# Kernel tuning notes

Measured on AMD Instinct MI355X. Metric: run time of the kernel, lower is better.

## Reference

```python
import jax, jax.numpy as jnp
import numpy as np

NUM_HEADS = 16


def setup_inputs() -> dict:
    key = jax.random.key(0)
    ks = jax.random.split(key, 5)
    B, L, D = 2, 2048, 1024
    x = jax.random.normal(ks[0], (B, L, D), dtype=jnp.float32)
    s = 1.0 / np.sqrt(D)
    Wqkv_w = jax.random.normal(ks[1], (3 * D, D), dtype=jnp.float32) * s
    Wqkv_b = jax.random.normal(ks[2], (3 * D,), dtype=jnp.float32) * 0.01
    out_w = jax.random.normal(ks[3], (D, D), dtype=jnp.float32) * s
    out_b = jax.random.normal(ks[4], (D,), dtype=jnp.float32) * 0.01
    return {"x": x, "Wqkv_w": Wqkv_w, "Wqkv_b": Wqkv_b, "out_w": out_w, "out_b": out_b}


def reference(x, Wqkv_w, Wqkv_b, out_w, out_b):
    B, L, D = x.shape
    H = NUM_HEADS
    d = D // H
    scale = 1.0 / np.sqrt(d).astype(np.float32)
    # qkv projection: torch Linear is x @ W^T + b
    qkv = x @ Wqkv_w.T + Wqkv_b                      # [B, L, 3D]
    qkv = qkv.reshape(B, L, 3, H, d)                 # (three h d) split
    qkv = jnp.transpose(qkv, (2, 0, 3, 1, 4))        # [3, B, H, L, d]
    q, k, v = qkv[0], qkv[1], qkv[2]
    k = k * scale
    # Linear-attention recurrence S_t = S_{t-1} + v_t k_t^T, y_t = S_t q_t
    # == causally-masked unnormalized attention: y_t = sum_{s<=t} (q_t.k_s) v_s
    scores = jnp.einsum('bhld,bhmd->bhlm', q, k)     # [B,H,L,L]
    causal = jnp.tril(jnp.ones((L, L), dtype=scores.dtype))
    y = jnp.einsum('bhlm,bhmd->bhld', scores * causal, v)  # [B,H,L,d]
    y = jnp.transpose(y, (0, 2, 1, 3)).reshape(B, L, D)    # b l (h d)
    return y @ out_w.T + out_b
```

## Files before the change

### kernel.cpp

```cpp
#include <hip/hip_runtime.h>


#define DEV __device__ __forceinline__

typedef __attribute__((ext_vector_type(8))) short bf16x8;
typedef __attribute__((ext_vector_type(4))) float f32x4;

DEV ushort f2bf(float f) {
  union { float f; unsigned u; } v; v.f = f;
  unsigned r = v.u + 0x7fffu + ((v.u >> 16) & 1u);
  return (ushort)(r >> 16);
}
DEV float bf2f(unsigned b) {
  union { unsigned u; float f; } v; v.u = (b & 0xffffu) << 16;
  return v.f;
}
DEV void glds16(const ushort* g, ushort* l) {
  __builtin_amdgcn_global_load_lds(
      (const __attribute__((address_space(1))) unsigned int*)g,
      (__attribute__((address_space(3))) unsigned int*)l, 16, 0, 0);
}

__global__ __launch_bounds__(256) void cvt_all(const float* __restrict__ x,
                                               const float* __restrict__ Ww,
                                               const float* __restrict__ Ow,
                                               ushort* __restrict__ xb,
                                               ushort* __restrict__ wqkvb,
                                               ushort* __restrict__ outwb) {
  int i = blockIdx.x * 256 + threadIdx.x;
  const float* src; ushort* dst; int off;
  if (i < 1048576)      { src = x;  dst = xb;    off = i; }
  else if (i < 1835008) { src = Ww; dst = wqkvb; off = i - 1048576; }
  else                  { src = Ow; dst = outwb; off = i - 1835008; }
  float4 v = ((const float4*)src)[off];
  ushort4 o;
  o.x = f2bf(v.x); o.y = f2bf(v.y); o.z = f2bf(v.z); o.w = f2bf(v.w);
  ((ushort4*)dst)[off] = o;
}

template <bool OUT_BF16, bool KSCALE>
__global__ __launch_bounds__(512, 2) void gemm_bt8(const ushort* __restrict__ A,
                                                   const ushort* __restrict__ Bw,
                                                   const float* __restrict__ bias,
                                                   void* __restrict__ Cout,
                                                   int M, int N, int K) {
  __shared__ __align__(16) ushort As[2][16384];
  __shared__ __align__(16) ushort Bs[2][16384];
  const int t = threadIdx.x;
  const int lane = t & 63, wid = t >> 6;
  const int quad = lane >> 4, l16 = lane & 15;
  const int wm2 = wid >> 2, wn4 = wid & 3;

  const int nwg = gridDim.x;
  const int bid = blockIdx.x;
  const int wg = (bid & 7) * (nwg >> 3) + (bid >> 3);
  const int nbx = N >> 8;
  const int bx = wg % nbx, by = wg / nbx;
  const int bm = by << 8, bn = bx << 8;

  const int srow = t >> 3;
  const int scol = ((t & 7) ^ (srow & 7)) << 3;
  const ushort* ag = A + (size_t)(bm + srow) * K + scol;
  const ushort* bg = Bw + (size_t)(bn + srow) * K + scol;
  const int NT = K >> 6;

  f32x4 acc[8][4];
  const f32x4 z = {0.f, 0.f, 0.f, 0.f};
#pragma unroll
  for (int i = 0; i < 8; ++i)
#pragma unroll
    for (int j = 0; j < 4; ++j) acc[i][j] = z;

  const int aRow = wm2 * 128 + l16;
  const int bRow = wn4 * 64 + l16;
  const int cxor = l16 & 7;

#define SG_A(bufi, kt, h, j) \
  glds16(ag + (size_t)((h)*128 + (j)*64) * K + ((kt) << 6), \
         &As[bufi][(h)*8192 + (j)*4096 + wid * 512])
#define SG_B(bufi, kt, h, j) \
  glds16(bg + (size_t)((h)*128 + (j)*64) * K + ((kt) << 6), \
         &Bs[bufi][(h)*8192 + (j)*4096 + wid * 512])
#define RD_A(bufi, mi, kc) \
  (*(const bf16x8*)&As[bufi][(aRow + (mi)*16) * 64 + ((((kc)*4 + quad) ^ cxor) << 3)])
#define RD_B(bufi, nj, kc) \
  (*(const bf16x8*)&Bs[bufi][(bRow + (nj)*16) * 64 + ((((kc)*4 + quad) ^ cxor) << 3)])

  SG_A(0, 0, 0, 0); SG_A(0, 0, 0, 1); SG_A(0, 0, 1, 0); SG_A(0, 0, 1, 1);
  SG_B(0, 0, 0, 0); SG_B(0, 0, 0, 1); SG_B(0, 0, 1, 0); SG_B(0, 0, 1, 1);
  asm volatile("s_waitcnt vmcnt(0)" ::: "memory");
  __builtin_amdgcn_s_barrier();

  bf16x8 bf[4][2], af[2][2];

#define LOAD_AF(rb, mi0) \
  af[0][0] = RD_A(rb, (mi0), 0); af[0][1] = RD_A(rb, (mi0), 1); \
  af[1][0] = RD_A(rb, (mi0) + 1, 0); af[1][1] = RD_A(rb, (mi0) + 1, 1);

#define MFMA16(mi0) \
  __builtin_amdgcn_s_setprio(1); \
  _Pragma("unroll") \
  for (int nj = 0; nj < 4; ++nj) { \
    acc[(mi0)][nj] = __builtin_amdgcn_mfma_f32_16x16x32_bf16(af[0][0], bf[nj][0], acc[(mi0)][nj], 0, 0, 0); \
    acc[(mi0)][nj] = __builtin_amdgcn_mfma_f32_16x16x32_bf16(af[0][1], bf[nj][1], acc[(mi0)][nj], 0, 0, 0); \
    acc[(mi0) + 1][nj] = __builtin_amdgcn_mfma_f32_16x16x32_bf16(af[1][0], bf[nj][0], acc[(mi0) + 1][nj], 0, 0, 0); \
    acc[(mi0) + 1][nj] = __builtin_amdgcn_mfma_f32_16x16x32_bf16(af[1][1], bf[nj][1], acc[(mi0) + 1][nj], 0, 0, 0); \
  } \
  __builtin_amdgcn_s_setprio(0);

#define HALFSTEP(rb, sb, stTile, doSt) do { \
    if (doSt) { SG_A(sb, stTile, 0, 0); SG_A(sb, stTile, 0, 1); \
                SG_A(sb, stTile, 1, 0); SG_A(sb, stTile, 1, 1); } \
    _Pragma("unroll") \
    for (int nj = 0; nj < 4; ++nj) { bf[nj][0] = RD_B(rb, nj, 0); bf[nj][1] = RD_B(rb, nj, 1); } \
    LOAD_AF(rb, 0); \
    __builtin_amdgcn_s_barrier(); \
    MFMA16(0); \
    __builtin_amdgcn_s_barrier(); \
    if (doSt) { SG_B(sb, stTile, 0, 0); SG_B(sb, stTile, 0, 1); } \
    LOAD_AF(rb, 2); \
    __builtin_amdgcn_s_barrier(); \
    MFMA16(2); \
    __builtin_amdgcn_s_barrier(); \
    if (doSt) { SG_B(sb, stTile, 1, 0); SG_B(sb, stTile, 1, 1); } \
    LOAD_AF(rb, 4); \
    __builtin_amdgcn_s_barrier(); \
    MFMA16(4); \
    __builtin_amdgcn_s_barrier(); \
    LOAD_AF(rb, 6); \
    __builtin_amdgcn_s_barrier(); \
    MFMA16(6); \
    asm volatile("s_waitcnt vmcnt(0)" ::: "memory"); \
    __builtin_amdgcn_s_barrier(); \
  } while (0)

  const int half = NT >> 1;
  for (int i = 0; i < half; ++i) {
    HALFSTEP(0, 1, 2 * i + 1, true);
    HALFSTEP(1, 0, 2 * i + 2, (i < half - 1));
  }

#undef HALFSTEP
#undef MFMA16
#undef LOAD_AF
#undef RD_A
#undef RD_B
#undef SG_A
#undef SG_B

#pragma unroll
  for (int mi = 0; mi < 8; ++mi)
#pragma unroll
    for (int nj = 0; nj < 4; ++nj) {
      const int col = bn + wn4 * 64 + nj * 16 + l16;
      const float bv = bias[col];
      float sc = 1.f;
      if (KSCALE) sc = ((col >> 10) == 1) ? 0.125f : 1.f;
#pragma unroll
      for (int r = 0; r < 4; ++r) {
        const int row = bm + wm2 * 128 + mi * 16 + quad * 4 + r;
        const float v = (acc[mi][nj][r] + bv) * sc;
        if (OUT_BF16)
          ((ushort*)Cout)[(size_t)row * N + col] = f2bf(v);
        else
          ((float*)Cout)[(size_t)row * N + col] = v;
      }
    }
}

__global__ __launch_bounds__(256) void gemm_out64(const ushort* __restrict__ A,
                                                  const ushort* __restrict__ Bw,
                                                  const float* __restrict__ bias,
                                                  float* __restrict__ C,
                                                  int M, int N, int K) {
  __shared__ ushort As[64 * 32];
  __shared__ ushort Bs[128 * 32];
  const int t = threadIdx.x;
  const int wid = t >> 6, lane = t & 63;
  const int quad = lane >> 4, l16 = lane & 15;
  const int bm = blockIdx.y * 64, bn = blockIdx.x * 128;
  const int wn = wid * 32;

  f32x4 acc[4][2];
  const f32x4 z = {0.f, 0.f, 0.f, 0.f};
#pragma unroll
  for (int i = 0; i < 4; ++i) { acc[i][0] = z; acc[i][1] = z; }

  const ushort* ag = A + (size_t)(bm + (t >> 2)) * K + ((t & 3) * 8);
  const ushort* bg = Bw + (size_t)(bn + (t >> 2)) * K + ((t & 3) * 8);
  ushort* asl = As + wid * 512;
  ushort* bsl = Bs + wid * 512;
  const size_t rowskip = (size_t)64 * K;

  for (int k0 = 0; k0 < K; k0 += 32) {
    glds16(ag + k0, asl);
    glds16(bg + k0, bsl);
    glds16(bg + k0 + rowskip, bsl + 2048);
    __syncthreads();
    bf16x8 af[4], bf[2];
#pragma unroll
    for (int i = 0; i < 4; ++i)
      af[i] = *(const bf16x8*)(As + (i * 16 + l16) * 32 + quad * 8);
#pragma unroll
    for (int j = 0; j < 2; ++j)
      bf[j] = *(const bf16x8*)(Bs + (wn + j * 16 + l16) * 32 + quad * 8);
#pragma unroll
    for (int i = 0; i < 4; ++i)
#pragma unroll
      for (int j = 0; j < 2; ++j)
        acc[i][j] = __builtin_amdgcn_mfma_f32_16x16x32_bf16(af[i], bf[j], acc[i][j], 0, 0, 0);
    __syncthreads();
  }

#pragma unroll
  for (int i = 0; i < 4; ++i)
#pragma unroll
    for (int j = 0; j < 2; ++j) {
      const int col = bn + wn + j * 16 + l16;
      const float bv = bias[col];
#pragma unroll
      for (int r = 0; r < 4; ++r) {
        const int row = bm + i * 16 + quad * 4 + r;
        C[(size_t)row * N + col] = acc[i][j][r] + bv;
      }
    }
}

__global__ __launch_bounds__(256) void kv_local(const ushort* __restrict__ qkv,
                                                float* __restrict__ mlocT) {
  const int c = blockIdx.x, bh = blockIdx.y;
  const int b = bh >> 4, hd = bh & 15;
  const int t = threadIdx.x;
  const int wid = t >> 6, lane = t & 63;
  const int quad = lane >> 4, l16 = lane & 15;
  __shared__ ushort kT[64 * 136];
  __shared__ ushort vT[64 * 136];

  {
    const int x = t & 127;
    const int isv = t >> 7;
    const int rp = x >> 1;
    const int half = (x & 1) * 32;
    const ushort* g0 = qkv + (size_t)(b * 2048 + c * 128 + 2 * rp) * 3072 +
                       1024 + isv * 1024 + hd * 64 + half;
    const ushort* g1 = g0 + 3072;
    ushort ta[32], tb[32];
#pragma unroll
    for (int q = 0; q < 4; ++q) {
      *(uint4*)(ta + q * 8) = *(const uint4*)(g0 + q * 8);
      *(uint4*)(tb + q * 8) = *(const uint4*)(g1 + q * 8);
    }
    ushort* dst = isv ? vT : kT;
#pragma unroll
    for (int j = 0; j < 32; ++j) {
      unsigned pk = (unsigned)ta[j] | ((unsigned)tb[j] << 16);
      *(unsigned*)(dst + (half + j) * 136 + 2 * rp) = pk;
    }
  }
  __syncthreads();

  const f32x4 z = {0.f, 0.f, 0.f, 0.f};
  f32x4 acc[4];
#pragma unroll
  for (int ct = 0; ct < 4; ++ct) acc[ct] = z;
#pragma unroll
  for (int kc = 0; kc < 4; ++kc) {
    bf16x8 afr = *(const bf16x8*)(vT + (wid * 16 + l16) * 136 + kc * 32 + quad * 8);
#pragma unroll
    for (int ct = 0; ct < 4; ++ct) {
      bf16x8 bfr = *(const bf16x8*)(kT + (ct * 16 + l16) * 136 + kc * 32 + quad * 8);
      acc[ct] = __builtin_amdgcn_mfma_f32_16x16x32_bf16(afr, bfr, acc[ct], 0, 0, 0);
    }
  }

  float* outp = mlocT + ((size_t)bh * 16 + c) * 4096;
#pragma unroll
  for (int ct = 0; ct < 4; ++ct)
#pragma unroll
    for (int r = 0; r < 4; ++r)
      outp[(wid * 16 + quad * 4 + r) * 64 + ct * 16 + l16] = acc[ct][r];
}

__global__ __launch_bounds__(256) void kv_prefix(const float* __restrict__ mlocT,
                                                 ushort* __restrict__ statesT) {
  const int slice = blockIdx.x, bh = blockIdx.y;
  const int eidx = slice * 256 + threadIdx.x;
  float run = 0.f;
  for (int c = 0; c < 16; ++c) {
    const size_t idx = ((size_t)bh * 16 + c) * 4096 + eidx;
    statesT[idx] = f2bf(run);
    run += mlocT[idx];
  }
}

__global__ __launch_bounds__(256) void attn_chunk(const ushort* __restrict__ qkv,
                                                  const ushort* __restrict__ statesT,
                                                  ushort* __restrict__ yb) {
  const int c = blockIdx.x, bh = blockIdx.y;
  const int b = bh >> 4, hd = bh & 15;
  const int l0 = c * 128;
  const int t = threadIdx.x;
  const int wid = t >> 6, lane = t & 63;
  const int quad = lane >> 4, l16 = lane & 15;

  __shared__ ushort P[16384];
  __shared__ ushort U[16384];
  ushort* Qs = U;
  ushort* Ks = U + 8192;
  ushort* vT = U;
  ushort* sT = U + 8704;

  {
    uint4 zz; zz.x = zz.y = zz.z = zz.w = 0u;
    uint4* p4 = (uint4*)P;
#pragma unroll
    for (int i = 0; i < 8; ++i) p4[i * 256 + t] = zz;
  }
  {
    const int kcs = ((lane & 7) ^ (lane >> 3)) * 8;
    const ushort* qg = qkv + (size_t)(b * 2048 + l0 + (t >> 3)) * 3072 + hd * 64 + kcs;
    ushort* ql = Qs + wid * 512;
    ushort* kl = Ks + wid * 512;
#pragma unroll
    for (int h2 = 0; h2 < 4; ++h2) {
      glds16(qg + (size_t)h2 * 32 * 3072, ql + h2 * 2048);
      glds16(qg + (size_t)h2 * 32 * 3072 + 1024, kl + h2 * 2048);
    }
  }
  __syncthreads();

  bf16x8 qf[2][2];
#pragma unroll
  for (int i = 0; i < 2; ++i) {
    const int rt = i ? (7 - wid) : wid;
#pragma unroll
    for (int kc = 0; kc < 2; ++kc)
      qf[i][kc] = *(const bf16x8*)(Qs + (rt * 16 + l16) * 64 +
                                   (((kc * 4 + quad) ^ (l16 & 7)) * 8));
  }

  const f32x4 z4 = {0.f, 0.f, 0.f, 0.f};
  f32x4 pacc[2][8];
#pragma unroll
  for (int i = 0; i < 2; ++i)
#pragma unroll
    for (int j = 0; j < 8; ++j) pacc[i][j] = z4;

#pragma unroll
  for (int i = 0; i < 2; ++i) {
    const int rt = i ? (7 - wid) : wid;
#pragma unroll
    for (int tj = 0; tj < 8; ++tj) {
      if (tj <= rt) {
#pragma unroll
        for (int kc = 0; kc < 2; ++kc) {
          bf16x8 kfr = *(const bf16x8*)(Ks + (tj * 16 + l16) * 64 +
                                        (((kc * 4 + quad) ^ (l16 & 7)) * 8));
          pacc[i][tj] = __builtin_amdgcn_mfma_f32_16x16x32_bf16(qf[i][kc], kfr, pacc[i][tj], 0, 0, 0);
        }
      }
    }
  }
  __syncthreads();

#pragma unroll
  for (int i = 0; i < 2; ++i) {
    const int rt = i ? (7 - wid) : wid;
#pragma unroll
    for (int tj = 0; tj < 8; ++tj) {
      if (tj <= rt) {
#pragma unroll
        for (int r = 0; r < 4; ++r) {
          const int row = rt * 16 + quad * 4 + r;
          const int scol = tj * 16 + l16;
          const float v = (scol <= row) ? pacc[i][tj][r] : 0.f;
          P[row * 128 + (((scol >> 3) ^ (row & 7)) * 8) + (scol & 7)] = f2bf(v);
        }
      }
    }
  }
  {
    const int p = t >> 2;
    const int eq = (t & 3) * 16;
    const ushort* vg0 = qkv + (size_t)(b * 2048 + l0 + 2 * p) * 3072 + 2048 + hd * 64 + eq;
    const ushort* vg1 = vg0 + 3072;
    ushort ta[16], tb[16];
    *(uint4*)(ta + 0) = *(const uint4*)(vg0 + 0);
    *(uint4*)(ta + 8) = *(const uint4*)(vg0 + 8);
    *(uint4*)(tb + 0) = *(const uint4*)(vg1 + 0);
    *(uint4*)(tb + 8) = *(const uint4*)(vg1 + 8);
#pragma unroll
    for (int j = 0; j < 16; ++j) {
      unsigned pk = (unsigned)ta[j] | ((unsigned)tb[j] << 16);
      *(unsigned*)(vT + (eq + j) * 136 + 2 * p) = pk;
    }
  }
  {
    const ushort* sg = statesT + ((size_t)bh * 16 + c) * 4096;
#pragma unroll
    for (int h = 0; h < 2; ++h) {
      const int cc = h * 256 + t;
      uint4 d = *(const uint4*)(sg + cc * 8);
      *(uint4*)(sT + (cc >> 3) * 72 + (cc & 7) * 8) = d;
    }
  }
  __syncthreads();

  f32x4 yacc[2][4];
#pragma unroll
  for (int i = 0; i < 2; ++i)
#pragma unroll
    for (int j = 0; j < 4; ++j) yacc[i][j] = z4;

#pragma unroll
  for (int i = 0; i < 2; ++i) {
    const int rt = i ? (7 - wid) : wid;
    const int kcmax = rt >> 1;
#pragma unroll
    for (int kc = 0; kc < 4; ++kc) {
      if (kc <= kcmax) {
        const int prow = rt * 16 + l16;
        bf16x8 pf;
        *(uint4*)&pf = *(const uint4*)(P + prow * 128 + (((kc * 4 + quad) ^ (prow & 7)) * 8));
#pragma unroll
        for (int ct = 0; ct < 4; ++ct) {
          bf16x8 vf = *(const bf16x8*)(vT + (ct * 16 + l16) * 136 + kc * 32 + quad * 8);
          yacc[i][ct] = __builtin_amdgcn_mfma_f32_16x16x32_bf16(pf, vf, yacc[i][ct], 0, 0, 0);
        }
      }
    }
#pragma unroll
    for (int kc = 0; kc < 2; ++kc) {
#pragma unroll
      for (int ct = 0; ct < 4; ++ct) {
        bf16x8 sf = *(const bf16x8*)(sT + (ct * 16 + l16) * 72 + kc * 32 + quad * 8);
        yacc[i][ct] = __builtin_amdgcn_mfma_f32_16x16x32_bf16(qf[i][kc], sf, yacc[i][ct], 0, 0, 0);
      }
    }
  }

#pragma unroll
  for (int i = 0; i < 2; ++i) {
    const int rt = i ? (7 - wid) : wid;
#pragma unroll
    for (int ct = 0; ct < 4; ++ct) {
#pragma unroll
      for (int r = 0; r < 4; ++r) {
        const int row = rt * 16 + quad * 4 + r;
        const int e = ct * 16 + l16;
        yb[(size_t)(b * 2048 + l0 + row) * 1024 + hd * 64 + e] = f2bf(yacc[i][ct][r]);
      }
    }
  }
}

extern "C" void kernel_launch(void* const* d_in, const int* in_sizes, int n_in,
                              void* d_out, int out_size, void* d_ws, size_t ws_size,
                              hipStream_t stream) {
  const float* x  = (const float*)d_in[0];
  const float* Ww = (const float*)d_in[1];
  const float* Wb = (const float*)d_in[2];
  const float* Ow = (const float*)d_in[3];
  const float* Ob = (const float*)d_in[4];
  float* out = (float*)d_out;

  char* ws = (char*)d_ws;
  ushort* xb      = (ushort*)(ws);
  ushort* wqkvb   = (ushort*)(ws + (size_t)8  * 1024 * 1024);
  ushort* outwb   = (ushort*)(ws + (size_t)14 * 1024 * 1024);
  ushort* qkvb    = (ushort*)(ws + (size_t)16 * 1024 * 1024);
  float*  mlocT   = (float*) (ws + (size_t)40 * 1024 * 1024);
  ushort* statesT = (ushort*)(ws + (size_t)48 * 1024 * 1024);
  ushort* yb      = (ushort*)(ws + (size_t)52 * 1024 * 1024);

  cvt_all<<<8192, 256, 0, stream>>>(x, Ww, Ow, xb, wqkvb, outwb);
  gemm_bt8<true, true><<<dim3(192), 512, 0, stream>>>(xb, wqkvb, Wb, (void*)qkvb, 4096, 3072, 1024);
  kv_local<<<dim3(16, 32), 256, 0, stream>>>(qkvb, mlocT);
  kv_prefix<<<dim3(16, 32), 256, 0, stream>>>(mlocT, statesT);
  attn_chunk<<<dim3(16, 32), 256, 0, stream>>>(qkvb, statesT, yb);
  gemm_out64<<<dim3(8, 64), 256, 0, stream>>>(yb, outwb, Ob, out, 4096, 1024, 1024);
}
```

Baseline: 160.0 us.

## Fuse fp32-to-bf16 conversion into GEMM tile loads, drop separate convert kernel

Removes the standalone cvt_all kernel. Both GEMMs now read fp32 inputs and weights directly from global memory into registers, pack them to bf16 with v_cvt_pk_bf16_f32, and write them into LDS. This saves one kernel launch plus the write and re-read of bf16 copies. In exchange, the async global_load_lds path becomes register-staged loads, which doubles the global bytes read per tile and adds register pressure in the main QKV GEMM pipeline.

New measurement: 176.0 us. 1.1x slower.

```diff
diff --git a/kernel.cpp b/kernel.cpp
--- a/kernel.cpp
+++ b/kernel.cpp
@@ -11,58 +11,40 @@
   unsigned r = v.u + 0x7fffu + ((v.u >> 16) & 1u);
   return (ushort)(r >> 16);
 }
-DEV float bf2f(unsigned b) {
-  union { unsigned u; float f; } v; v.u = (b & 0xffffu) << 16;
-  return v.f;
-}
 DEV void glds16(const ushort* g, ushort* l) {
   __builtin_amdgcn_global_load_lds(
       (const __attribute__((address_space(1))) unsigned int*)g,
       (__attribute__((address_space(3))) unsigned int*)l, 16, 0, 0);
 }
-
-__global__ __launch_bounds__(256) void cvt_all(const float* __restrict__ x,
-                                               const float* __restrict__ Ww,
-                                               const float* __restrict__ Ow,
-                                               ushort* __restrict__ xb,
-                                               ushort* __restrict__ wqkvb,
-                                               ushort* __restrict__ outwb) {
-  int i = blockIdx.x * 256 + threadIdx.x;
-  const float* src; ushort* dst; int off;
-  if (i < 1048576)      { src = x;  dst = xb;    off = i; }
-  else if (i < 1835008) { src = Ww; dst = wqkvb; off = i - 1048576; }
-  else                  { src = Ow; dst = outwb; off = i - 1835008; }
-  float4 v = ((const float4*)src)[off];
-  ushort4 o;
-  o.x = f2bf(v.x); o.y = f2bf(v.y); o.z = f2bf(v.z); o.w = f2bf(v.w);
-  ((ushort4*)dst)[off] = o;
-}
-
-template <bool OUT_BF16, bool KSCALE>
-__global__ __launch_bounds__(512, 2) void gemm_bt8(const ushort* __restrict__ A,
-                                                   const ushort* __restrict__ Bw,
-                                                   const float* __restrict__ bias,
-                                                   void* __restrict__ Cout,
-                                                   int M, int N, int K) {
+DEV uint4 pk8(float4 a, float4 b) {
+  uint4 o;
+  asm("v_cvt_pk_bf16_f32 %0, %1, %2" : "=v"(o.x) : "v"(a.x), "v"(a.y));
+  asm("v_cvt_pk_bf16_f32 %0, %1, %2" : "=v"(o.y) : "v"(a.z), "v"(a.w));
+  asm("v_cvt_pk_bf16_f32 %0, %1, %2" : "=v"(o.z) : "v"(b.x), "v"(b.y));
+  asm("v_cvt_pk_bf16_f32 %0, %1, %2" : "=v"(o.w) : "v"(b.z), "v"(b.w));
+  return o;
+}
+
+__global__ __launch_bounds__(512, 2) void gemm_qkv_f32(const float* __restrict__ Af,
+                                                       const float* __restrict__ Bf,
+                                                       const float* __restrict__ bias,
+                                                       ushort* __restrict__ Cout) {
   __shared__ __align__(16) ushort As[2][16384];
   __shared__ __align__(16) ushort Bs[2][16384];
+  const int K = 1024, N = 3072;
   const int t = threadIdx.x;
   const int lane = t & 63, wid = t >> 6;
   const int quad = lane >> 4, l16 = lane & 15;
   const int wm2 = wid >> 2, wn4 = wid & 3;
 
-  const int nwg = gridDim.x;
   const int bid = blockIdx.x;
-  const int wg = (bid & 7) * (nwg >> 3) + (bid >> 3);
-  const int nbx = N >> 8;
-  const int bx = wg % nbx, by = wg / nbx;
+  const int wg = (bid & 7) * 24 + (bid >> 3);
+  const int bx = wg % 12, by = wg / 12;
   const int bm = by << 8, bn = bx << 8;
 
   const int srow = t >> 3;
-  const int scol = ((t & 7) ^ (srow & 7)) << 3;
-  const ushort* ag = A + (size_t)(bm + srow) * K + scol;
-  const ushort* bg = Bw + (size_t)(bn + srow) * K + scol;
-  const int NT = K >> 6;
+  const int scolf = ((t & 7) ^ (srow & 7)) << 3;
+  const int wdst = wid * 512 + lane * 8;
 
   f32x4 acc[8][4];
   const f32x4 z = {0.f, 0.f, 0.f, 0.f};
@@ -75,21 +57,35 @@
   const int bRow = wn4 * 64 + l16;
   const int cxor = l16 & 7;
 
-#define SG_A(bufi, kt, h, j) \
-  glds16(ag + (size_t)((h)*128 + (j)*64) * K + ((kt) << 6), \
-         &As[bufi][(h)*8192 + (j)*4096 + wid * 512])
-#define SG_B(bufi, kt, h, j) \
-  glds16(bg + (size_t)((h)*128 + (j)*64) * K + ((kt) << 6), \
-         &Bs[bufi][(h)*8192 + (j)*4096 + wid * 512])
+#define LD_A(kt, h, j, r0, r1) { \
+    const float* p_ = Af + (size_t)(bm + (h)*128 + (j)*64 + srow) * K + scolf + ((kt) << 6); \
+    r0 = *(const float4*)p_; r1 = *(const float4*)(p_ + 4); }
+#define LD_B(kt, h, j, r0, r1) { \
+    const float* p_ = Bf + (size_t)(bn + (h)*128 + (j)*64 + srow) * K + scolf + ((kt) << 6); \
+    r0 = *(const float4*)p_; r1 = *(const float4*)(p_ + 4); }
+#define ST_A(bufi, h, j, r0, r1) \
+    *(uint4*)&As[bufi][(h)*8192 + (j)*4096 + wdst] = pk8(r0, r1);
+#define ST_B(bufi, h, j, r0, r1) \
+    *(uint4*)&Bs[bufi][(h)*8192 + (j)*4096 + wdst] = pk8(r0, r1);
 #define RD_A(bufi, mi, kc) \
   (*(const bf16x8*)&As[bufi][(aRow + (mi)*16) * 64 + ((((kc)*4 + quad) ^ cxor) << 3)])
 #define RD_B(bufi, nj, kc) \
   (*(const bf16x8*)&Bs[bufi][(bRow + (nj)*16) * 64 + ((((kc)*4 + quad) ^ cxor) << 3)])
 
-  SG_A(0, 0, 0, 0); SG_A(0, 0, 0, 1); SG_A(0, 0, 1, 0); SG_A(0, 0, 1, 1);
-  SG_B(0, 0, 0, 0); SG_B(0, 0, 0, 1); SG_B(0, 0, 1, 0); SG_B(0, 0, 1, 1);
-  asm volatile("s_waitcnt vmcnt(0)" ::: "memory");
-  __builtin_amdgcn_s_barrier();
+  {
+    float4 a0, a1, a2, a3, a4, a5, a6, a7;
+    float4 b0, b1, b2, b3, b4, b5, b6, b7;
+    LD_A(0, 0, 0, a0, a1); LD_A(0, 0, 1, a2, a3);
+    LD_A(0, 1, 0, a4, a5); LD_A(0, 1, 1, a6, a7);
+    LD_B(0, 0, 0, b0, b1); LD_B(0, 0, 1, b2, b3);
+    LD_B(0, 1, 0, b4, b5); LD_B(0, 1, 1, b6, b7);
+    ST_A(0, 0, 0, a0, a1); ST_A(0, 0, 1, a2, a3);
+    ST_A(0, 1, 0, a4, a5); ST_A(0, 1, 1, a6, a7);
+    ST_B(0, 0, 0, b0, b1); ST_B(0, 0, 1, b2, b3);
+    ST_B(0, 1, 0, b4, b5); ST_B(0, 1, 1, b6, b7);
+    asm volatile("s_waitcnt lgkmcnt(0)" ::: "memory");
+    __builtin_amdgcn_s_barrier();
+  }
 
   bf16x8 bf[4][2], af[2][2];
 
@@ -109,20 +105,26 @@
   __builtin_amdgcn_s_setprio(0);
 
 #define HALFSTEP(rb, sb, stTile, doSt) do { \
-    if (doSt) { SG_A(sb, stTile, 0, 0); SG_A(sb, stTile, 0, 1); \
-                SG_A(sb, stTile, 1, 0); SG_A(sb, stTile, 1, 1); } \
+    float4 a0, a1, a2, a3, a4, a5, a6, a7; \
+    float4 b0, b1, b2, b3, b4, b5, b6, b7; \
+    if (doSt) { LD_A(stTile, 0, 0, a0, a1); LD_A(stTile, 0, 1, a2, a3); \
+                LD_A(stTile, 1, 0, a4, a5); LD_A(stTile, 1, 1, a6, a7); } \
     _Pragma("unroll") \
     for (int nj = 0; nj < 4; ++nj) { bf[nj][0] = RD_B(rb, nj, 0); bf[nj][1] = RD_B(rb, nj, 1); } \
     LOAD_AF(rb, 0); \
     __builtin_amdgcn_s_barrier(); \
     MFMA16(0); \
     __builtin_amdgcn_s_barrier(); \
-    if (doSt) { SG_B(sb, stTile, 0, 0); SG_B(sb, stTile, 0, 1); } \
+    if (doSt) { LD_B(stTile, 0, 0, b0, b1); LD_B(stTile, 0, 1, b2, b3); \
+                LD_B(stTile, 1, 0, b4, b5); LD_B(stTile, 1, 1, b6, b7); \
+                ST_A(sb, 0, 0, a0, a1); ST_A(sb, 0, 1, a2, a3); \
+                ST_A(sb, 1, 0, a4, a5); ST_A(sb, 1, 1, a6, a7); } \
     LOAD_AF(rb, 2); \
     __builtin_amdgcn_s_barrier(); \
     MFMA16(2); \
     __builtin_amdgcn_s_barrier(); \
-    if (doSt) { SG_B(sb, stTile, 1, 0); SG_B(sb, stTile, 1, 1); } \
+    if (doSt) { ST_B(sb, 0, 0, b0, b1); ST_B(sb, 0, 1, b2, b3); \
+                ST_B(sb, 1, 0, b4, b5); ST_B(sb, 1, 1, b6, b7); } \
     LOAD_AF(rb, 4); \
     __builtin_amdgcn_s_barrier(); \
     MFMA16(4); \
@@ -130,14 +132,13 @@
     LOAD_AF(rb, 6); \
     __builtin_amdgcn_s_barrier(); \
     MFMA16(6); \
-    asm volatile("s_waitcnt vmcnt(0)" ::: "memory"); \
+    asm volatile("s_waitcnt lgkmcnt(0)" ::: "memory"); \
     __builtin_amdgcn_s_barrier(); \
   } while (0)
 
-  const int half = NT >> 1;
-  for (int i = 0; i < half; ++i) {
+  for (int i = 0; i < 8; ++i) {
     HALFSTEP(0, 1, 2 * i + 1, true);
-    HALFSTEP(1, 0, 2 * i + 2, (i < half - 1));
+    HALFSTEP(1, 0, 2 * i + 2, (i < 7));
   }
 
 #undef HALFSTEP
@@ -145,8 +146,10 @@
 #undef LOAD_AF
 #undef RD_A
 #undef RD_B
-#undef SG_A
-#undef SG_B
+#undef ST_A
+#undef ST_B
+#undef LD_A
+#undef LD_B
 
 #pragma unroll
   for (int mi = 0; mi < 8; ++mi)
@@ -154,25 +157,20 @@
     for (int nj = 0; nj < 4; ++nj) {
       const int col = bn + wn4 * 64 + nj * 16 + l16;
       const float bv = bias[col];
-      float sc = 1.f;
-      if (KSCALE) sc = ((col >> 10) == 1) ? 0.125f : 1.f;
+      const float sc = ((col >> 10) == 1) ? 0.125f : 1.f;
 #pragma unroll
       for (int r = 0; r < 4; ++r) {
         const int row = bm + wm2 * 128 + mi * 16 + quad * 4 + r;
-        const float v = (acc[mi][nj][r] + bv) * sc;
-        if (OUT_BF16)
-          ((ushort*)Cout)[(size_t)row * N + col] = f2bf(v);
-        else
-          ((float*)Cout)[(size_t)row * N + col] = v;
-      }
-    }
-}
-
-__global__ __launch_bounds__(256) void gemm_out64(const ushort* __restrict__ A,
-                                                  const ushort* __restrict__ Bw,
-                                                  const float* __restrict__ bias,
-                                                  float* __restrict__ C,
-                                                  int M, int N, int K) {
+        Cout[(size_t)row * N + col] = f2bf((acc[mi][nj][r] + bv) * sc);
+      }
+    }
+}
+
+__global__ __launch_bounds__(256) void gemm_out64f(const ushort* __restrict__ A,
+                                                   const float* __restrict__ Bf,
+                                                   const float* __restrict__ bias,
+                                                   float* __restrict__ C,
+                                                   int M, int N, int K) {
   __shared__ ushort As[64 * 32];
   __shared__ ushort Bs[128 * 32];
   const int t = threadIdx.x;
@@ -187,28 +185,34 @@
   for (int i = 0; i < 4; ++i) { acc[i][0] = z; acc[i][1] = z; }
 
   const ushort* ag = A + (size_t)(bm + (t >> 2)) * K + ((t & 3) * 8);
-  const ushort* bg = Bw + (size_t)(bn + (t >> 2)) * K + ((t & 3) * 8);
+  const float* bgf = Bf + (size_t)(bn + (t >> 2)) * K + ((t & 3) * 8);
   ushort* asl = As + wid * 512;
-  ushort* bsl = Bs + wid * 512;
-  const size_t rowskip = (size_t)64 * K;
+  const int bw = wid * 512 + lane * 8;
+  const size_t rowskipf = (size_t)64 * K;
 
   for (int k0 = 0; k0 < K; k0 += 32) {
     glds16(ag + k0, asl);
-    glds16(bg + k0, bsl);
-    glds16(bg + k0 + rowskip, bsl + 2048);
+    {
+      const float* p0 = bgf + k0;
+      const float* p1 = bgf + k0 + rowskipf;
+      float4 c0 = *(const float4*)p0, c1 = *(const float4*)(p0 + 4);
+      float4 c2 = *(const float4*)p1, c3 = *(const float4*)(p1 + 4);
+      *(uint4*)&Bs[bw] = pk8(c0, c1);
+      *(uint4*)&Bs[2048 + bw] = pk8(c2, c3);
+    }
     __syncthreads();
-    bf16x8 af[4], bf[2];
+    bf16x8 af[4], bff[2];
 #pragma unroll
     for (int i = 0; i < 4; ++i)
       af[i] = *(const bf16x8*)(As + (i * 16 + l16) * 32 + quad * 8);
 #pragma unroll
     for (int j = 0; j < 2; ++j)
-      bf[j] = *(const bf16x8*)(Bs + (wn + j * 16 + l16) * 32 + quad * 8);
+      bff[j] = *(const bf16x8*)(Bs + (wn + j * 16 + l16) * 32 + quad * 8);
 #pragma unroll
     for (int i = 0; i < 4; ++i)
 #pragma unroll
       for (int j = 0; j < 2; ++j)
-        acc[i][j] = __builtin_amdgcn_mfma_f32_16x16x32_bf16(af[i], bf[j], acc[i][j], 0, 0, 0);
+        acc[i][j] = __builtin_amdgcn_mfma_f32_16x16x32_bf16(af[i], bff[j], acc[i][j], 0, 0, 0);
     __syncthreads();
   }
 
@@ -465,18 +469,14 @@
   float* out = (float*)d_out;
 
   char* ws = (char*)d_ws;
-  ushort* xb      = (ushort*)(ws);
-  ushort* wqkvb   = (ushort*)(ws + (size_t)8  * 1024 * 1024);
-  ushort* outwb   = (ushort*)(ws + (size_t)14 * 1024 * 1024);
   ushort* qkvb    = (ushort*)(ws + (size_t)16 * 1024 * 1024);
   float*  mlocT   = (float*) (ws + (size_t)40 * 1024 * 1024);
   ushort* statesT = (ushort*)(ws + (size_t)48 * 1024 * 1024);
   ushort* yb      = (ushort*)(ws + (size_t)52 * 1024 * 1024);
 
-  cvt_all<<<8192, 256, 0, stream>>>(x, Ww, Ow, xb, wqkvb, outwb);
-  gemm_bt8<true, true><<<dim3(192), 512, 0, stream>>>(xb, wqkvb, Wb, (void*)qkvb, 4096, 3072, 1024);
+  gemm_qkv_f32<<<dim3(192), 512, 0, stream>>>(x, Ww, Wb, qkvb);
   kv_local<<<dim3(16, 32), 256, 0, stream>>>(qkvb, mlocT);
   kv_prefix<<<dim3(16, 32), 256, 0, stream>>>(mlocT, statesT);
   attn_chunk<<<dim3(16, 32), 256, 0, stream>>>(qkvb, statesT, yb);
-  gemm_out64<<<dim3(8, 64), 256, 0, stream>>>(yb, outwb, Ob, out, 4096, 1024, 1024);
-}
+  gemm_out64f<<<dim3(8, 64), 256, 0, stream>>>(yb, Ow, Ob, out, 4096, 1024, 1024);
+}
```

## Fuse kv_local, kv_prefix and attn_chunk into one cooperative kernel with grid syncs

Applied to the files above, without the earlier changes.

Merges the three middle kernels (per-chunk KV state, prefix scan over chunks, chunked attention) into a single cooperative launch separated by two grid-wide syncs. The goal is to remove two kernel launch gaps and their tail effects. Shared memory is unified into one 64KB buffer reused across phases, with launch bounds asking for 2 blocks per CU so all 512 blocks can be co-resident. Grid syncs cost time themselves, and cooperative launch can fail if residency isn't met.

Result: slower. 285.4 us (+78.4%).

```diff
diff --git a/kernel.cpp b/kernel.cpp
--- a/kernel.cpp
+++ b/kernel.cpp
@@ -1,7 +1,10 @@
 #include <hip/hip_runtime.h>
+#include <hip/hip_cooperative_groups.h>
 
 
 #define DEV __device__ __forceinline__
+
+namespace cg = cooperative_groups;
 
 typedef __attribute__((ext_vector_type(8))) short bf16x8;
 typedef __attribute__((ext_vector_type(4))) float f32x4;
@@ -10,10 +13,6 @@
   union { float f; unsigned u; } v; v.f = f;
   unsigned r = v.u + 0x7fffu + ((v.u >> 16) & 1u);
   return (ushort)(r >> 16);
-}
-DEV float bf2f(unsigned b) {
-  union { unsigned u; float f; } v; v.u = (b & 0xffffu) << 16;
-  return v.f;
 }
 DEV void glds16(const ushort* g, ushort* l) {
   __builtin_amdgcn_global_load_lds(
@@ -226,229 +225,229 @@
     }
 }
 
-__global__ __launch_bounds__(256) void kv_local(const ushort* __restrict__ qkv,
-                                                float* __restrict__ mlocT) {
+__global__ __launch_bounds__(256, 2) void mid_fused(const ushort* __restrict__ qkv,
+                                                    float* __restrict__ mlocT,
+                                                    ushort* __restrict__ statesT,
+                                                    ushort* __restrict__ yb) {
+  cg::grid_group grid = cg::this_grid();
   const int c = blockIdx.x, bh = blockIdx.y;
   const int b = bh >> 4, hd = bh & 15;
   const int t = threadIdx.x;
   const int wid = t >> 6, lane = t & 63;
   const int quad = lane >> 4, l16 = lane & 15;
-  __shared__ ushort kT[64 * 136];
-  __shared__ ushort vT[64 * 136];
+
+  __shared__ __align__(16) ushort SH[32768];
 
   {
-    const int x = t & 127;
-    const int isv = t >> 7;
-    const int rp = x >> 1;
-    const int half = (x & 1) * 32;
-    const ushort* g0 = qkv + (size_t)(b * 2048 + c * 128 + 2 * rp) * 3072 +
-                       1024 + isv * 1024 + hd * 64 + half;
-    const ushort* g1 = g0 + 3072;
-    ushort ta[32], tb[32];
-#pragma unroll
-    for (int q = 0; q < 4; ++q) {
-      *(uint4*)(ta + q * 8) = *(const uint4*)(g0 + q * 8);
-      *(uint4*)(tb + q * 8) = *(const uint4*)(g1 + q * 8);
-    }
-    ushort* dst = isv ? vT : kT;
-#pragma unroll
-    for (int j = 0; j < 32; ++j) {
-      unsigned pk = (unsigned)ta[j] | ((unsigned)tb[j] << 16);
-      *(unsigned*)(dst + (half + j) * 136 + 2 * rp) = pk;
-    }
-  }
-  __syncthreads();
-
-  const f32x4 z = {0.f, 0.f, 0.f, 0.f};
-  f32x4 acc[4];
-#pragma unroll
-  for (int ct = 0; ct < 4; ++ct) acc[ct] = z;
-#pragma unroll
-  for (int kc = 0; kc < 4; ++kc) {
-    bf16x8 afr = *(const bf16x8*)(vT + (wid * 16 + l16) * 136 + kc * 32 + quad * 8);
-#pragma unroll
-    for (int ct = 0; ct < 4; ++ct) {
-      bf16x8 bfr = *(const bf16x8*)(kT + (ct * 16 + l16) * 136 + kc * 32 + quad * 8);
-      acc[ct] = __builtin_amdgcn_mfma_f32_16x16x32_bf16(afr, bfr, acc[ct], 0, 0, 0);
-    }
-  }
-
-  float* outp = mlocT + ((size_t)bh * 16 + c) * 4096;
-#pragma unroll
-  for (int ct = 0; ct < 4; ++ct)
-#pragma unroll
-    for (int r = 0; r < 4; ++r)
-      outp[(wid * 16 + quad * 4 + r) * 64 + ct * 16 + l16] = acc[ct][r];
-}
-
-__global__ __launch_bounds__(256) void kv_prefix(const float* __restrict__ mlocT,
-                                                 ushort* __restrict__ statesT) {
-  const int slice = blockIdx.x, bh = blockIdx.y;
-  const int eidx = slice * 256 + threadIdx.x;
-  float run = 0.f;
-  for (int c = 0; c < 16; ++c) {
-    const size_t idx = ((size_t)bh * 16 + c) * 4096 + eidx;
-    statesT[idx] = f2bf(run);
-    run += mlocT[idx];
-  }
-}
-
-__global__ __launch_bounds__(256) void attn_chunk(const ushort* __restrict__ qkv,
-                                                  const ushort* __restrict__ statesT,
-                                                  ushort* __restrict__ yb) {
-  const int c = blockIdx.x, bh = blockIdx.y;
-  const int b = bh >> 4, hd = bh & 15;
-  const int l0 = c * 128;
-  const int t = threadIdx.x;
-  const int wid = t >> 6, lane = t & 63;
-  const int quad = lane >> 4, l16 = lane & 15;
-
-  __shared__ ushort P[16384];
-  __shared__ ushort U[16384];
-  ushort* Qs = U;
-  ushort* Ks = U + 8192;
-  ushort* vT = U;
-  ushort* sT = U + 8704;
+    ushort* kT = SH;
+    ushort* vT = SH + 8704;
+    {
+      const int x = t & 127;
+      const int isv = t >> 7;
+      const int rp = x >> 1;
+      const int half = (x & 1) * 32;
+      const ushort* g0 = qkv + (size_t)(b * 2048 + c * 128 + 2 * rp) * 3072 +
+                         1024 + isv * 1024 + hd * 64 + half;
+      const ushort* g1 = g0 + 3072;
+      ushort ta[32], tb[32];
+#pragma unroll
+      for (int q = 0; q < 4; ++q) {
+        *(uint4*)(ta + q * 8) = *(const uint4*)(g0 + q * 8);
+        *(uint4*)(tb + q * 8) = *(const uint4*)(g1 + q * 8);
+      }
+      ushort* dst = isv ? vT : kT;
+#pragma unroll
+      for (int j = 0; j < 32; ++j) {
+        unsigned pk = (unsigned)ta[j] | ((unsigned)tb[j] << 16);
+        *(unsigned*)(dst + (half + j) * 136 + 2 * rp) = pk;
+      }
+    }
+    __syncthreads();
+
+    const f32x4 z = {0.f, 0.f, 0.f, 0.f};
+    f32x4 acc[4];
+#pragma unroll
+    for (int ct = 0; ct < 4; ++ct) acc[ct] = z;
+#pragma unroll
+    for (int kc = 0; kc < 4; ++kc) {
+      bf16x8 afr = *(const bf16x8*)(vT + (wid * 16 + l16) * 136 + kc * 32 + quad * 8);
+#pragma unroll
+      for (int ct = 0; ct < 4; ++ct) {
+        bf16x8 bfr = *(const bf16x8*)(kT + (ct * 16 + l16) * 136 + kc * 32 + quad * 8);
+        acc[ct] = __builtin_amdgcn_mfma_f32_16x16x32_bf16(afr, bfr, acc[ct], 0, 0, 0);
+      }
+    }
+    float* outp = mlocT + ((size_t)bh * 16 + c) * 4096;
+#pragma unroll
+    for (int ct = 0; ct < 4; ++ct)
+#pragma unroll
+      for (int r = 0; r < 4; ++r)
+        outp[(wid * 16 + quad * 4 + r) * 64 + ct * 16 + l16] = acc[ct][r];
+  }
+
+  grid.sync();
 
   {
-    uint4 zz; zz.x = zz.y = zz.z = zz.w = 0u;
-    uint4* p4 = (uint4*)P;
-#pragma unroll
-    for (int i = 0; i < 8; ++i) p4[i * 256 + t] = zz;
-  }
+    const int eidx = c * 256 + t;
+    float run = 0.f;
+    for (int cc = 0; cc < 16; ++cc) {
+      const size_t idx = ((size_t)bh * 16 + cc) * 4096 + eidx;
+      statesT[idx] = f2bf(run);
+      run += mlocT[idx];
+    }
+  }
+
+  grid.sync();
+
   {
-    const int kcs = ((lane & 7) ^ (lane >> 3)) * 8;
-    const ushort* qg = qkv + (size_t)(b * 2048 + l0 + (t >> 3)) * 3072 + hd * 64 + kcs;
-    ushort* ql = Qs + wid * 512;
-    ushort* kl = Ks + wid * 512;
-#pragma unroll
-    for (int h2 = 0; h2 < 4; ++h2) {
-      glds16(qg + (size_t)h2 * 32 * 3072, ql + h2 * 2048);
-      glds16(qg + (size_t)h2 * 32 * 3072 + 1024, kl + h2 * 2048);
-    }
-  }
-  __syncthreads();
-
-  bf16x8 qf[2][2];
-#pragma unroll
-  for (int i = 0; i < 2; ++i) {
-    const int rt = i ? (7 - wid) : wid;
-#pragma unroll
-    for (int kc = 0; kc < 2; ++kc)
-      qf[i][kc] = *(const bf16x8*)(Qs + (rt * 16 + l16) * 64 +
-                                   (((kc * 4 + quad) ^ (l16 & 7)) * 8));
-  }
-
-  const f32x4 z4 = {0.f, 0.f, 0.f, 0.f};
-  f32x4 pacc[2][8];
-#pragma unroll
-  for (int i = 0; i < 2; ++i)
-#pragma unroll
-    for (int j = 0; j < 8; ++j) pacc[i][j] = z4;
-
-#pragma unroll
-  for (int i = 0; i < 2; ++i) {
-    const int rt = i ? (7 - wid) : wid;
-#pragma unroll
-    for (int tj = 0; tj < 8; ++tj) {
-      if (tj <= rt) {
-#pragma unroll
-        for (int kc = 0; kc < 2; ++kc) {
-          bf16x8 kfr = *(const bf16x8*)(Ks + (tj * 16 + l16) * 64 +
-                                        (((kc * 4 + quad) ^ (l16 & 7)) * 8));
-          pacc[i][tj] = __builtin_amdgcn_mfma_f32_16x16x32_bf16(qf[i][kc], kfr, pacc[i][tj], 0, 0, 0);
+    const int l0 = c * 128;
+    ushort* P = SH;
+    ushort* U = SH + 16384;
+    ushort* Qs = U;
+    ushort* Ks = U + 8192;
+    ushort* vT = U;
+    ushort* sT = U + 8704;
+
+    {
+      uint4 zz; zz.x = zz.y = zz.z = zz.w = 0u;
+      uint4* p4 = (uint4*)P;
+#pragma unroll
+      for (int i = 0; i < 8; ++i) p4[i * 256 + t] = zz;
+    }
+    {
+      const int kcs = ((lane & 7) ^ (lane >> 3)) * 8;
+      const ushort* qg = qkv + (size_t)(b * 2048 + l0 + (t >> 3)) * 3072 + hd * 64 + kcs;
+      ushort* ql = Qs + wid * 512;
+      ushort* kl = Ks + wid * 512;
+#pragma unroll
+      for (int h2 = 0; h2 < 4; ++h2) {
+        glds16(qg + (size_t)h2 * 32 * 3072, ql + h2 * 2048);
+        glds16(qg + (size_t)h2 * 32 * 3072 + 1024, kl + h2 * 2048);
+      }
+    }
+    __syncthreads();
+
+    bf16x8 qf[2][2];
+#pragma unroll
+    for (int i = 0; i < 2; ++i) {
+      const int rt = i ? (7 - wid) : wid;
+#pragma unroll
+      for (int kc = 0; kc < 2; ++kc)
+        qf[i][kc] = *(const bf16x8*)(Qs + (rt * 16 + l16) * 64 +
+                                     (((kc * 4 + quad) ^ (l16 & 7)) * 8));
+    }
+
+    const f32x4 z4 = {0.f, 0.f, 0.f, 0.f};
+    f32x4 pacc[2][8];
+#pragma unroll
+    for (int i = 0; i < 2; ++i)
+#pragma unroll
+      for (int j = 0; j < 8; ++j) pacc[i][j] = z4;
+
+#pragma unroll
+    for (int i = 0; i < 2; ++i) {
+      const int rt = i ? (7 - wid) : wid;
+#pragma unroll
+      for (int tj = 0; tj < 8; ++tj) {
+        if (tj <= rt) {
+#pragma unroll
+          for (int kc = 0; kc < 2; ++kc) {
+            bf16x8 kfr = *(const bf16x8*)(Ks + (tj * 16 + l16) * 64 +
+                                          (((kc * 4 + quad) ^ (l16 & 7)) * 8));
+            pacc[i][tj] = __builtin_amdgcn_mfma_f32_16x16x32_bf16(qf[i][kc], kfr, pacc[i][tj], 0, 0, 0);
+          }
         }
       }
     }
-  }
-  __syncthreads();
-
-#pragma unroll
-  for (int i = 0; i < 2; ++i) {
-    const int rt = i ? (7 - wid) : wid;
-#pragma unroll
-    for (int tj = 0; tj < 8; ++tj) {
-      if (tj <= rt) {
+    __syncthreads();
+
+#pragma unroll
+    for (int i = 0; i < 2; ++i) {
+      const int rt = i ? (7 - wid) : wid;
+#pragma unroll
+      for (int tj = 0; tj < 8; ++tj) {
+        if (tj <= rt) {
+#pragma unroll
+          for (int r = 0; r < 4; ++r) {
+            const int row = rt * 16 + quad * 4 + r;
+            const int scol = tj * 16 + l16;
+            const float v = (scol <= row) ? pacc[i][tj][r] : 0.f;
+            P[row * 128 + (((scol >> 3) ^ (row & 7)) * 8) + (scol & 7)] = f2bf(v);
+          }
+        }
+      }
+    }
+    {
+      const int p = t >> 2;
+      const int eq = (t & 3) * 16;
+      const ushort* vg0 = qkv + (size_t)(b * 2048 + l0 + 2 * p) * 3072 + 2048 + hd * 64 + eq;
+      const ushort* vg1 = vg0 + 3072;
+      ushort ta[16], tb[16];
+      *(uint4*)(ta + 0) = *(const uint4*)(vg0 + 0);
+      *(uint4*)(ta + 8) = *(const uint4*)(vg0 + 8);
+      *(uint4*)(tb + 0) = *(const uint4*)(vg1 + 0);
+      *(uint4*)(tb + 8) = *(const uint4*)(vg1 + 8);
+#pragma unroll
+      for (int j = 0; j < 16; ++j) {
+        unsigned pk = (unsigned)ta[j] | ((unsigned)tb[j] << 16);
+        *(unsigned*)(vT + (eq + j) * 136 + 2 * p) = pk;
+      }
+    }
+    {
+      const ushort* sg = statesT + ((size_t)bh * 16 + c) * 4096;
+#pragma unroll
+      for (int h = 0; h < 2; ++h) {
+        const int cc2 = h * 256 + t;
+        uint4 d = *(const uint4*)(sg + cc2 * 8);
+        *(uint4*)(sT + (cc2 >> 3) * 72 + (cc2 & 7) * 8) = d;
+      }
+    }
+    __syncthreads();
+
+    f32x4 yacc[2][4];
+#pragma unroll
+    for (int i = 0; i < 2; ++i)
+#pragma unroll
+      for (int j = 0; j < 4; ++j) yacc[i][j] = z4;
+
+#pragma unroll
+    for (int i = 0; i < 2; ++i) {
+      const int rt = i ? (7 - wid) : wid;
+      const int kcmax = rt >> 1;
+#pragma unroll
+      for (int kc = 0; kc < 4; ++kc) {
+        if (kc <= kcmax) {
+          const int prow = rt * 16 + l16;
+          bf16x8 pf;
+          *(uint4*)&pf = *(const uint4*)(P + prow * 128 + (((kc * 4 + quad) ^ (prow & 7)) * 8));
+#pragma unroll
+          for (int ct = 0; ct < 4; ++ct) {
+            bf16x8 vf = *(const bf16x8*)(vT + (ct * 16 + l16) * 136 + kc * 32 + quad * 8);
+            yacc[i][ct] = __builtin_amdgcn_mfma_f32_16x16x32_bf16(pf, vf, yacc[i][ct], 0, 0, 0);
+          }
+        }
+      }
+#pragma unroll
+      for (int kc = 0; kc < 2; ++kc) {
+#pragma unroll
+        for (int ct = 0; ct < 4; ++ct) {
+          bf16x8 sf = *(const bf16x8*)(sT + (ct * 16 + l16) * 72 + kc * 32 + quad * 8);
+          yacc[i][ct] = __builtin_amdgcn_mfma_f32_16x16x32_bf16(qf[i][kc], sf, yacc[i][ct], 0, 0, 0);
+        }
+      }
+    }
+
+#pragma unroll
+    for (int i = 0; i < 2; ++i) {
+      const int rt = i ? (7 - wid) : wid;
+#pragma unroll
+      for (int ct = 0; ct < 4; ++ct) {
 #pragma unroll
         for (int r = 0; r < 4; ++r) {
           const int row = rt * 16 + quad * 4 + r;
-          const int scol = tj * 16 + l16;
-          const float v = (scol <= row) ? pacc[i][tj][r] : 0.f;
-          P[row * 128 + (((scol >> 3) ^ (row & 7)) * 8) + (scol & 7)] = f2bf(v);
+          const int e = ct * 16 + l16;
+          yb[(size_t)(b * 2048 + l0 + row) * 1024 + hd * 64 + e] = f2bf(yacc[i][ct][r]);
         }
-      }
-    }
-  }
-  {
-    const int p = t >> 2;
-    const int eq = (t & 3) * 16;
-    const ushort* vg0 = qkv + (size_t)(b * 2048 + l0 + 2 * p) * 3072 + 2048 + hd * 64 + eq;
-    const ushort* vg1 = vg0 + 3072;
-    ushort ta[16], tb[16];
-    *(uint4*)(ta + 0) = *(const uint4*)(vg0 + 0);
-    *(uint4*)(ta + 8) = *(const uint4*)(vg0 + 8);
-    *(uint4*)(tb + 0) = *(const uint4*)(vg1 + 0);
-    *(uint4*)(tb + 8) = *(const uint4*)(vg1 + 8);
-#pragma unroll
-    for (int j = 0; j < 16; ++j) {
-      unsigned pk = (unsigned)ta[j] | ((unsigned)tb[j] << 16);
-      *(unsigned*)(vT + (eq + j) * 136 + 2 * p) = pk;
-    }
-  }
-  {
-    const ushort* sg = statesT + ((size_t)bh * 16 + c) * 4096;
-#pragma unroll
-    for (int h = 0; h < 2; ++h) {
-      const int cc = h * 256 + t;
-      uint4 d = *(const uint4*)(sg + cc * 8);
-      *(uint4*)(sT + (cc >> 3) * 72 + (cc & 7) * 8) = d;
-    }
-  }
-  __syncthreads();
-
-  f32x4 yacc[2][4];
-#pragma unroll
-  for (int i = 0; i < 2; ++i)
-#pragma unroll
-    for (int j = 0; j < 4; ++j) yacc[i][j] = z4;
-
-#pragma unroll
-  for (int i = 0; i < 2; ++i) {
-    const int rt = i ? (7 - wid) : wid;
-    const int kcmax = rt >> 1;
-#pragma unroll
-    for (int kc = 0; kc < 4; ++kc) {
-      if (kc <= kcmax) {
-        const int prow = rt * 16 + l16;
-        bf16x8 pf;
-        *(uint4*)&pf = *(const uint4*)(P + prow * 128 + (((kc * 4 + quad) ^ (prow & 7)) * 8));
-#pragma unroll
-        for (int ct = 0; ct < 4; ++ct) {
-          bf16x8 vf = *(const bf16x8*)(vT + (ct * 16 + l16) * 136 + kc * 32 + quad * 8);
-          yacc[i][ct] = __builtin_amdgcn_mfma_f32_16x16x32_bf16(pf, vf, yacc[i][ct], 0, 0, 0);
-        }
-      }
-    }
-#pragma unroll
-    for (int kc = 0; kc < 2; ++kc) {
-#pragma unroll
-      for (int ct = 0; ct < 4; ++ct) {
-        bf16x8 sf = *(const bf16x8*)(sT + (ct * 16 + l16) * 72 + kc * 32 + quad * 8);
-        yacc[i][ct] = __builtin_amdgcn_mfma_f32_16x16x32_bf16(qf[i][kc], sf, yacc[i][ct], 0, 0, 0);
-      }
-    }
-  }
-
-#pragma unroll
-  for (int i = 0; i < 2; ++i) {
-    const int rt = i ? (7 - wid) : wid;
-#pragma unroll
-    for (int ct = 0; ct < 4; ++ct) {
-#pragma unroll
-      for (int r = 0; r < 4; ++r) {
-        const int row = rt * 16 + quad * 4 + r;
-        const int e = ct * 16 + l16;
-        yb[(size_t)(b * 2048 + l0 + row) * 1024 + hd * 64 + e] = f2bf(yacc[i][ct][r]);
       }
     }
   }
@@ -475,8 +474,10 @@
 
   cvt_all<<<8192, 256, 0, stream>>>(x, Ww, Ow, xb, wqkvb, outwb);
   gemm_bt8<true, true><<<dim3(192), 512, 0, stream>>>(xb, wqkvb, Wb, (void*)qkvb, 4096, 3072, 1024);
-  kv_local<<<dim3(16, 32), 256, 0, stream>>>(qkvb, mlocT);
-  kv_prefix<<<dim3(16, 32), 256, 0, stream>>>(mlocT, statesT);
-  attn_chunk<<<dim3(16, 32), 256, 0, stream>>>(qkvb, statesT, yb);
+  {
+    void* args[] = {(void*)&qkvb, (void*)&mlocT, (void*)&statesT, (void*)&yb};
+    hipLaunchCooperativeKernel((const void*)mid_fused, dim3(16, 32), dim3(256),
+                               args, 0, stream);
+  }
   gemm_out64<<<dim3(8, 64), 256, 0, stream>>>(yb, outwb, Ob, out, 4096, 1024, 1024);
 }
```
